# Kernel tuning notes

Hardware: AMD Instinct MI355X
Metric: run time of the kernel (lower is better)

The kernel has to match this reference:

```python
import jax, jax.numpy as jnp
import numpy as np

NUM_HEADS = 8
WINDOW = 64
ENCODERS = 6
EPS = 1e-5


def _positional_encoding(S, D, dtype=jnp.float32):
    pos = jnp.arange(S, dtype=jnp.float32)[:, None]
    div = jnp.exp(-jnp.log(10000.0) * jnp.arange(0, D, 2, dtype=jnp.float32) / D)
    ang = pos * div  # [S, D/2]
    pe = jnp.zeros((S, D), dtype=jnp.float32)
    pe = pe.at[:, 0::2].set(jnp.sin(ang)).at[:, 1::2].set(jnp.cos(ang))
    return pe.astype(dtype)


def _layernorm(x, g, b):
    mu = jnp.mean(x, axis=-1, keepdims=True)
    var = jnp.var(x, axis=-1, keepdims=True)
    return (x - mu) * jax.lax.rsqrt(var + EPS) * g + b


def _local_attention(x, wq, bq, wk, bk, wv, bv, window_mask):
    B, S, D = x.shape
    Dh = D // NUM_HEADS
    scale = Dh ** -0.5
    def split(t):  # [B,S,D] -> [B,H,S,Dh]
        return t.reshape(B, S, NUM_HEADS, Dh).transpose(0, 2, 1, 3)
    q = split(x @ wq.T + bq)
    k = split(x @ wk.T + bk)
    v = split(x @ wv.T + bv)
    scores = jnp.einsum('bhqd,bhkd->bhqk', q, k)
    # FAITHFUL: out-of-window entries are ZERO (not -inf); softmax over full S.
    scores = jnp.where(window_mask, scores, 0.0) * scale
    probs = jax.nn.softmax(scores, axis=-1)
    out = jnp.einsum('bhqk,bhkd->bhqd', probs, v)
    return out.transpose(0, 2, 1, 3).reshape(B, S, D)


def reference(inputs, emb, wq, bq, wk, bk, wv, bv, ln_g, ln_b,
              fc1_w, fc1_b, fc2_w, fc2_b, out_w, out_b):
    B, S = inputs.shape
    D = emb.shape[1]
    # window slice in torch source: [max(0, i-W), min(S, i+W))  (end exclusive)
    i = jnp.arange(S)[:, None]
    j = jnp.arange(S)[None, :]
    window_mask = (j >= i - WINDOW) & (j < i + WINDOW)  # [S, S]

    x = emb[inputs]  # [B, S, D]
    x = x + _positional_encoding(S, D, x.dtype)
    for _ in range(ENCODERS):  # shared weights across encoder iterations
        a = _local_attention(x, wq, bq, wk, bk, wv, bv, window_mask)
        x = _layernorm(a, ln_g, ln_b)
        h = jax.nn.relu(x @ fc1_w.T + fc1_b)
        x = (h @ fc2_w.T + fc2_b) + x
        x = _layernorm(x, ln_g, ln_b)
    x = x.reshape(B, S * D)
    return x @ out_w.T + out_b


def setup_inputs() -> dict:
    key = jax.random.key(0)
    ks = jax.random.split(key, 16)
    B, S, D, Hd, V, C = 8, 1024, 512, 2048, 32000, 6
    s = 0.02
    return {
        'inputs': jax.random.randint(ks[0], (B, S), 0, 31999),
        'emb': jax.random.normal(ks[1], (V, D), jnp.float32) * s,
        'wq': jax.random.normal(ks[2], (D, D), jnp.float32) * s,
        'bq': jnp.zeros((D,), jnp.float32),
        'wk': jax.random.normal(ks[3], (D, D), jnp.float32) * s,
        'bk': jnp.zeros((D,), jnp.float32),
        'wv': jax.random.normal(ks[4], (D, D), jnp.float32) * s,
        'bv': jnp.zeros((D,), jnp.float32),
        'ln_g': jnp.ones((D,), jnp.float32),
        'ln_b': jnp.zeros((D,), jnp.float32),
        'fc1_w': jax.random.normal(ks[5], (Hd, D), jnp.float32) * s,
        'fc1_b': jnp.zeros((Hd,), jnp.float32),
        'fc2_w': jax.random.normal(ks[6], (D, Hd), jnp.float32) * s,
        'fc2_b': jnp.zeros((D,), jnp.float32),
        'out_w': jax.random.normal(ks[7], (C, S * D), jnp.float32) * s,
        'out_b': jnp.zeros((C,), jnp.float32),
    }
```

## Files before the change

### kernel.cpp

```cpp
#include <hip/hip_runtime.h>

#define S_LEN 1024
#define DMODEL 512
#define NHEADS 8
#define DHEAD 64
#define HDIM 2048
#define WIN 64

typedef _Float16 f16x8 __attribute__((ext_vector_type(8)));
typedef _Float16 f16x2 __attribute__((ext_vector_type(2)));
typedef float f32x4 __attribute__((ext_vector_type(4)));
typedef float f32x16 __attribute__((ext_vector_type(16)));

__device__ __forceinline__ void stage16(const _Float16* g, _Float16* l) {
  __builtin_amdgcn_global_load_lds((const __attribute__((address_space(1))) unsigned int*)g,
                                   (__attribute__((address_space(3))) unsigned int*)l, 16, 0, 0);
}

__global__ void wprep_kernel(const float* __restrict__ wq, const float* __restrict__ wk,
                             const float* __restrict__ wv, const float* __restrict__ bq,
                             const float* __restrict__ bk, const float* __restrict__ bv,
                             const float* __restrict__ w1, const float* __restrict__ w2,
                             const float* __restrict__ wo,
                             _Float16* __restrict__ Wqkv, float* __restrict__ bqkv,
                             _Float16* __restrict__ W1h, _Float16* __restrict__ W2h,
                             _Float16* __restrict__ Woh) {
  int i = blockIdx.x * 256 + threadIdx.x;
  if (i < 262144) {
    Wqkv[i]          = (_Float16)wq[i];
    Wqkv[262144 + i] = (_Float16)wk[i];
    Wqkv[524288 + i] = (_Float16)wv[i];
  }
  if (i < 1048576) {
    W1h[i] = (_Float16)w1[i];
    W2h[i] = (_Float16)w2[i];
    Woh[i]           = (_Float16)wo[i];
    Woh[1048576 + i] = (_Float16)wo[1048576 + i];
    Woh[2097152 + i] = (_Float16)wo[2097152 + i];
  }
  if (i < 512) { bqkv[i] = bq[i]; bqkv[512 + i] = bk[i]; bqkv[1024 + i] = bv[i]; }
}

__global__ void embed_pe_kernel(const int* __restrict__ inputs, const float* __restrict__ emb,
                                _Float16* __restrict__ Xb) {
  int row = blockIdx.x;
  int s = row & (S_LEN - 1);
  int t = threadIdx.x;
  int tok = inputs[row];
  float dv = __expf(-logf(10000.0f) * (2.0f * (float)t) / (float)DMODEL);
  float ang = (float)s * dv;
  float sv = sinf(ang);
  float cv = cosf(ang);
  size_t base = (size_t)row * DMODEL + 2 * t;
  float x0 = emb[(size_t)tok * DMODEL + 2 * t] + sv;
  float x1 = emb[(size_t)tok * DMODEL + 2 * t + 1] + cv;
  f16x2 h; h[0] = (_Float16)x0; h[1] = (_Float16)x1;
  *(f16x2*)(Xb + base) = h;
}

#define EPI_RELU16 1
#define EPI_QKV 3
#define EPI_PART 4

template <int EPI>
__launch_bounds__(256)
__global__ void mfma_gemm(const _Float16* __restrict__ A, const _Float16* __restrict__ W,
                          const float* __restrict__ bias,
                          float* __restrict__ Cf0, float* __restrict__ Cf1,
                          _Float16* __restrict__ Ch, float* __restrict__ VS,
                          int M, int N, int Kstride, int Kslice) {
  __shared__ _Float16 As[2][128 * 32];
  __shared__ _Float16 Bs[2][128 * 32];
  const int bm = blockIdx.x * 128;
  const int bn = blockIdx.y * 128;
  const int z = blockIdx.z;
  const int t = threadIdx.x;
  const int lane = t & 63;
  const int w = t >> 6;
  const int wr = w >> 1, wc = w & 1;
  const int l15 = lane & 15, l4 = lane >> 4;

  const int idx0 = t, idx1 = t + 256;
  const int r0 = idx0 >> 2, kg0 = (idx0 & 3) << 3;
  const int r1 = idx1 >> 2, kg1 = (idx1 & 3) << 3;
  const _Float16* Ag0 = A + (size_t)(bm + r0) * Kstride + kg0;
  const _Float16* Ag1 = A + (size_t)(bm + r1) * Kstride + kg1;
  const _Float16* Wg0 = W + (size_t)(bn + r0) * Kstride + kg0;
  const _Float16* Wg1 = W + (size_t)(bn + r1) * Kstride + kg1;

  const int kbeg = z * Kslice;
  const int nsteps = Kslice >> 5;

  stage16(Ag0 + kbeg, As[0] + idx0 * 8);
  stage16(Ag1 + kbeg, As[0] + idx1 * 8);
  stage16(Wg0 + kbeg, Bs[0] + idx0 * 8);
  stage16(Wg1 + kbeg, Bs[0] + idx1 * 8);
  __syncthreads();

  f32x4 acc[4][4] = {};
  int cur = 0;
  for (int s = 0; s < nsteps; ++s) {
    if (s + 1 < nsteps) {
      int kn = kbeg + (s + 1) * 32;
      stage16(Ag0 + kn, As[cur ^ 1] + idx0 * 8);
      stage16(Ag1 + kn, As[cur ^ 1] + idx1 * 8);
      stage16(Wg0 + kn, Bs[cur ^ 1] + idx0 * 8);
      stage16(Wg1 + kn, Bs[cur ^ 1] + idx1 * 8);
    }
    f16x8 af[4], bf[4];
#pragma unroll
    for (int m = 0; m < 4; ++m)
      af[m] = *(const f16x8*)&As[cur][(wr * 64 + m * 16 + l15) * 32 + l4 * 8];
#pragma unroll
    for (int n = 0; n < 4; ++n)
      bf[n] = *(const f16x8*)&Bs[cur][(wc * 64 + n * 16 + l15) * 32 + l4 * 8];
#pragma unroll
    for (int m = 0; m < 4; ++m)
#pragma unroll
      for (int n = 0; n < 4; ++n)
        acc[m][n] = __builtin_amdgcn_mfma_f32_16x16x32_f16(af[m], bf[n], acc[m][n], 0, 0, 0);
    __syncthreads();
    cur ^= 1;
  }

  float* dst = (EPI == EPI_PART) ? (z ? Cf1 : Cf0) : Cf0;
  float cs[4] = {0.f, 0.f, 0.f, 0.f};
#pragma unroll
  for (int n = 0; n < 4; ++n) {
    int col = bn + wc * 64 + n * 16 + l15;
    float bb = (EPI == EPI_PART) ? 0.f : bias[col];
#pragma unroll
    for (int m = 0; m < 4; ++m) {
      int row = bm + wr * 64 + m * 16 + l4 * 4;
#pragma unroll
      for (int j = 0; j < 4; ++j) {
        float v = acc[m][n][j] + bb;
        if (EPI == EPI_RELU16) {
          v = fmaxf(v, 0.0f);
          Ch[(size_t)(row + j) * N + col] = (_Float16)v;
        } else if (EPI == EPI_QKV) {
          Ch[(size_t)(row + j) * N + col] = (_Float16)v;
          cs[n] += v;
        } else {
          dst[(size_t)(row + j) * N + col] = v;
        }
      }
    }
  }
  if (EPI == EPI_QKV && bn >= 1024) {
    const int batch = bm >> 10;
#pragma unroll
    for (int n = 0; n < 4; ++n) {
      float s = cs[n];
      s += __shfl_xor(s, 16);
      s += __shfl_xor(s, 32);
      if (l4 == 0) {
        int col = bn + wc * 64 + n * 16 + l15;
        atomicAdd(&VS[batch * 512 + (col - 1024)], s);
      }
    }
  }
}

__global__ void vs_zero_kernel(float* __restrict__ VS) {
  VS[blockIdx.x * 256 + threadIdx.x] = 0.0f;
}

#define KTMAX 256
#define VTS 264

__launch_bounds__(256)
__global__ void attn_kernel(const _Float16* __restrict__ QKVh, const float* __restrict__ VSg,
                            float* __restrict__ O) {
  __shared__ _Float16 Ks[KTMAX * 64];
  __shared__ _Float16 Vt[64 * VTS];
  __shared__ float VsC[8][64];

  const int qb0 = blockIdx.x * 128, h = blockIdx.y, b = blockIdx.z;
  const int jlo = max(0, qb0 - WIN);
  const int jhi = min(S_LEN, qb0 + 128 + WIN);
  const int KT = jhi - jlo;
  const int t = threadIdx.x;
  const int lane = t & 63, w = t >> 6;
  const int hi = lane >> 5, l31 = lane & 31;

  const _Float16* Kg = QKVh + ((size_t)(b * S_LEN + jlo)) * 1536 + 512 + h * 64;
#pragma unroll
  for (int p = 0; p < 8; ++p) {
    int u = t + p * 256;
    int row = u >> 3;
    int cb = (u & 7) * 16;
    int rowc = min(row, KT - 1);
    int scb = cb ^ ((row & 7) << 4);
    stage16(Kg + (size_t)rowc * 1536 + (scb >> 1), Ks + u * 8);
  }
  const _Float16* Vg = QKVh + ((size_t)(b * S_LEN + jlo)) * 1536 + 1024 + h * 64;
#pragma unroll
  for (int p = 0; p < 8; ++p) {
    int u = t + p * 256;
    int row = u >> 3;
    int d0 = (u & 7) * 8;
    f16x8 v = {0, 0, 0, 0, 0, 0, 0, 0};
    if (row < KT) v = *(const f16x8*)(Vg + (size_t)row * 1536 + d0);
#pragma unroll
    for (int e = 0; e < 8; ++e) Vt[(d0 + e) * VTS + row] = v[e];
  }
  __syncthreads();
  for (int slot = t; slot < 512; slot += 256) {
    int c = slot >> 6, d = slot & 63;
    const f16x8* col = (const f16x8*)(Vt + d * VTS + c * 32);
    float s = 0.f;
#pragma unroll
    for (int g = 0; g < 4; ++g) {
      f16x8 v = col[g];
#pragma unroll
      for (int e = 0; e < 8; ++e) s += (float)v[e];
    }
    VsC[c][d] = s;
  }
  const int qw = qb0 + w * 32;
  const _Float16* Qg = QKVh + ((size_t)(b * S_LEN + qw + l31)) * 1536 + h * 64;
  f16x8 qf[4];
#pragma unroll
  for (int ds = 0; ds < 4; ++ds) qf[ds] = *(const f16x8*)(Qg + ds * 16 + hi * 8);
  __syncthreads();

  const int c0 = max(0, qw - WIN - jlo) >> 5;
  const int c1 = min(KT, qw + 96 - jlo) >> 5;
  const int nproc = (c1 - c0) * 32;
  const int i = qw + l31;
  const int wlo = i - WIN, whi = i + WIN;

  float m = 0.f, l = 0.f;
  f32x16 accA = {}, accB = {};

  union PK { f16x2 h; unsigned u; };
  union A8 { unsigned u[4]; f16x8 h; };

  for (int c = c0; c < c1; ++c) {
    const int kb = c * 32;
    f32x16 sf = {};
#pragma unroll
    for (int ds = 0; ds < 4; ++ds) {
      int row = kb + l31;
      int cbyte = ((ds * 16 + hi * 8) * 2) ^ ((row & 7) << 4);
      f16x8 kf = *(const f16x8*)((const char*)Ks + row * 128 + cbyte);
      sf = __builtin_amdgcn_mfma_f32_32x32x16_f16(kf, qf[ds], sf, 0, 0, 0);
    }
    float s[16]; float pm = -1e30f;
#pragma unroll
    for (int r = 0; r < 16; ++r) {
      int gk = jlo + kb + (r & 3) + 8 * (r >> 2) + 4 * hi;
      float v = (gk >= wlo && gk < whi) ? sf[r] * 0.125f : 0.f;
      s[r] = v;
      pm = fmaxf(pm, v);
    }
    pm = fmaxf(pm, __shfl_xor(pm, 32));
    if (!__all(pm <= m + 8.f)) {
      float mn = fmaxf(m, pm);
      float f = __expf(m - mn);
      l *= f;
#pragma unroll
      for (int r = 0; r < 16; ++r) {
        int q = (r & 3) + 8 * (r >> 2) + 4 * hi;
        float fr = __shfl(f, q);
        accA[r] *= fr; accB[r] *= fr;
      }
      m = mn;
    }
    float p[16]; float ls = 0.f;
#pragma unroll
    for (int r = 0; r < 16; ++r) { p[r] = __expf(s[r] - m); ls += p[r]; }
    l += ls;
    unsigned u[8], x[8];
#pragma unroll
    for (int kk = 0; kk < 8; ++kk) {
      PK cv; cv.h[0] = (_Float16)p[2 * kk]; cv.h[1] = (_Float16)p[2 * kk + 1];
      u[kk] = cv.u;
    }
#pragma unroll
    for (int kk = 0; kk < 8; ++kk) x[kk] = (unsigned)__shfl_xor((int)u[kk], 32);
    A8 a0, a1;
    a0.u[0] = hi ? x[2] : u[0]; a0.u[1] = hi ? x[3] : u[1];
    a0.u[2] = hi ? u[2] : x[0]; a0.u[3] = hi ? u[3] : x[1];
    a1.u[0] = hi ? x[6] : u[4]; a1.u[1] = hi ? x[7] : u[5];
    a1.u[2] = hi ? u[6] : x[4]; a1.u[3] = hi ? u[7] : x[5];
#pragma unroll
    for (int ks = 0; ks < 2; ++ks) {
      f16x8 pa = ks ? a1.h : a0.h;
      f16x8 v0 = *(const f16x8*)(Vt + (size_t)(l31) * VTS + kb + ks * 16 + hi * 8);
      f16x8 v1 = *(const f16x8*)(Vt + (size_t)(32 + l31) * VTS + kb + ks * 16 + hi * 8);
      accA = __builtin_amdgcn_mfma_f32_32x32x16_f16(pa, v0, accA, 0, 0, 0);
      accB = __builtin_amdgcn_mfma_f32_32x32x16_f16(pa, v1, accB, 0, 0, 0);
    }
  }

  l = l + __shfl_xor(l, 32);
  const int dA = l31, dB = 32 + l31;
  float vsA = 0.f, vsB = 0.f;
  for (int c = c0; c < c1; ++c) { vsA += VsC[c][dA]; vsB += VsC[c][dB]; }
  const float vtA = VSg[b * 512 + h * 64 + dA];
  const float vtB = VSg[b * 512 + h * 64 + dB];
  const float zcount = (float)(S_LEN - nproc);
#pragma unroll
  for (int r = 0; r < 16; ++r) {
    int q = (r & 3) + 8 * (r >> 2) + 4 * hi;
    float mq = __shfl(m, q);
    float lq = __shfl(l, q);
    float em = __expf(-mq);
    float denom = lq + zcount * em;
    float inv = 1.0f / denom;
    size_t rowbase = ((size_t)(b * S_LEN + qw + q)) * DMODEL + h * 64;
    O[rowbase + dA] = (accA[r] + em * (vtA - vsA)) * inv;
    O[rowbase + dB] = (accB[r] + em * (vtB - vsB)) * inv;
  }
}

__global__ void ln_kernel(const float* __restrict__ X, const float* __restrict__ g,
                          const float* __restrict__ be, float* __restrict__ Y,
                          _Float16* __restrict__ Yh) {
  int row = blockIdx.x;
  int t = threadIdx.x;
  const float* x = X + (size_t)row * DMODEL;
  float2 v = *(const float2*)(x + 2 * t);
  float s = v.x + v.y;
  float sq = v.x * v.x + v.y * v.y;
#pragma unroll
  for (int off = 32; off; off >>= 1) {
    s += __shfl_xor(s, off);
    sq += __shfl_xor(sq, off);
  }
  __shared__ float ss[4], sqq[4];
  int w = t >> 6, lane = t & 63;
  if (lane == 0) { ss[w] = s; sqq[w] = sq; }
  __syncthreads();
  s = ss[0] + ss[1] + ss[2] + ss[3];
  sq = sqq[0] + sqq[1] + sqq[2] + sqq[3];
  float mu = s * (1.0f / DMODEL);
  float var = sq * (1.0f / DMODEL) - mu * mu;
  float rstd = rsqrtf(var + 1e-5f);
  float g0 = g[2 * t], g1 = g[2 * t + 1];
  float b0 = be[2 * t], b1 = be[2 * t + 1];
  float2 o;
  o.x = (v.x - mu) * rstd * g0 + b0;
  o.y = (v.y - mu) * rstd * g1 + b1;
  *(float2*)(Y + (size_t)row * DMODEL + 2 * t) = o;
  f16x2 hh; hh[0] = (_Float16)o.x; hh[1] = (_Float16)o.y;
  *(f16x2*)(Yh + (size_t)row * DMODEL + 2 * t) = hh;
}

__global__ void ln2_fused_kernel(const float* __restrict__ P0, const float* __restrict__ P1,
                                 const float* __restrict__ XB, const float* __restrict__ fb,
                                 const float* __restrict__ g, const float* __restrict__ be,
                                 _Float16* __restrict__ Yh) {
  int row = blockIdx.x;
  int t = threadIdx.x;
  size_t off = (size_t)row * DMODEL + 2 * t;
  float2 p0 = *(const float2*)(P0 + off);
  float2 p1 = *(const float2*)(P1 + off);
  float2 xb = *(const float2*)(XB + off);
  float2 v;
  v.x = p0.x + p1.x + fb[2 * t]     + xb.x;
  v.y = p0.y + p1.y + fb[2 * t + 1] + xb.y;
  float s = v.x + v.y;
  float sq = v.x * v.x + v.y * v.y;
#pragma unroll
  for (int off2 = 32; off2; off2 >>= 1) {
    s += __shfl_xor(s, off2);
    sq += __shfl_xor(sq, off2);
  }
  __shared__ float ss[4], sqq[4];
  int w = t >> 6, lane = t & 63;
  if (lane == 0) { ss[w] = s; sqq[w] = sq; }
  __syncthreads();
  s = ss[0] + ss[1] + ss[2] + ss[3];
  sq = sqq[0] + sqq[1] + sqq[2] + sqq[3];
  float mu = s * (1.0f / DMODEL);
  float var = sq * (1.0f / DMODEL) - mu * mu;
  float rstd = rsqrtf(var + 1e-5f);
  float g0 = g[2 * t], g1 = g[2 * t + 1];
  float b0 = be[2 * t], b1 = be[2 * t + 1];
  f16x2 hh;
  hh[0] = (_Float16)((v.x - mu) * rstd * g0 + b0);
  hh[1] = (_Float16)((v.y - mu) * rstd * g1 + b1);
  *(f16x2*)(Yh + off) = hh;
}

__global__ void outproj_partial_kernel(const _Float16* __restrict__ Xb,
                                       const _Float16* __restrict__ Woh,
                                       float* __restrict__ part) {
  const int KTOT = S_LEN * DMODEL;
  const int CH = KTOT / 32;
  int chunk = blockIdx.x, c = blockIdx.y, b = blockIdx.z;
  const int t = threadIdx.x;
  const _Float16* x = Xb + (size_t)b * KTOT + (size_t)chunk * CH;
  const _Float16* wv = Woh + (size_t)c * KTOT + (size_t)chunk * CH;
  float acc = 0.f;
#pragma unroll
  for (int p = 0; p < 8; ++p) {
    f16x8 a = *(const f16x8*)(x + (p * 256 + t) * 8);
    f16x8 w8 = *(const f16x8*)(wv + (p * 256 + t) * 8);
#pragma unroll
    for (int e = 0; e < 8; ++e) acc += (float)a[e] * (float)w8[e];
  }
#pragma unroll
  for (int off = 32; off; off >>= 1) acc += __shfl_xor(acc, off);
  __shared__ float red[4];
  int w = t >> 6, lane = t & 63;
  if (lane == 0) red[w] = acc;
  __syncthreads();
  if (t == 0)
    part[(b * 6 + c) * 32 + chunk] = red[0] + red[1] + red[2] + red[3];
}

__global__ void outproj_final_kernel(const float* __restrict__ part, const float* __restrict__ ob,
                                     float* __restrict__ out) {
  int idx = threadIdx.x;
  if (idx < 48) {
    float s = 0.f;
#pragma unroll
    for (int k = 0; k < 32; ++k) s += part[idx * 32 + k];
    out[idx] = s + ob[idx % 6];
  }
}

extern "C" void kernel_launch(void* const* d_in, const int* in_sizes, int n_in,
                              void* d_out, int out_size, void* d_ws, size_t ws_size,
                              hipStream_t stream) {
  (void)in_sizes; (void)n_in; (void)out_size; (void)ws_size;
  const int*   inputs = (const int*)  d_in[0];
  const float* emb    = (const float*)d_in[1];
  const float* wq     = (const float*)d_in[2];
  const float* bq     = (const float*)d_in[3];
  const float* wk     = (const float*)d_in[4];
  const float* bk     = (const float*)d_in[5];
  const float* wv     = (const float*)d_in[6];
  const float* bv     = (const float*)d_in[7];
  const float* ln_g   = (const float*)d_in[8];
  const float* ln_b   = (const float*)d_in[9];
  const float* fc1_w  = (const float*)d_in[10];
  const float* fc1_b  = (const float*)d_in[11];
  const float* fc2_w  = (const float*)d_in[12];
  const float* fc2_b  = (const float*)d_in[13];
  const float* out_w  = (const float*)d_in[14];
  const float* out_b  = (const float*)d_in[15];
  float* out = (float*)d_out;

  const int M = 8192;
  char* p = (char*)d_ws;
  float*    P0   = (float*)p;      p += (size_t)M * 512 * 4;
  _Float16* Xb   = (_Float16*)p;   p += (size_t)M * 512 * 2;
  _Float16* QKVh = (_Float16*)p;   p += (size_t)M * 1536 * 2;
  float*    XB   = (float*)p;      p += (size_t)M * 512 * 4;
  _Float16* XBb  = (_Float16*)p;   p += (size_t)M * 512 * 2;
  _Float16* H    = (_Float16*)p;   p += (size_t)M * 2048 * 2;
  float*    Ab   = (float*)H;
  _Float16* Wqkv = (_Float16*)p;   p += (size_t)1536 * 512 * 2;
  _Float16* W1h  = (_Float16*)p;   p += (size_t)2048 * 512 * 2;
  _Float16* W2h  = (_Float16*)p;   p += (size_t)512 * 2048 * 2;
  _Float16* Woh  = (_Float16*)p;   p += (size_t)6 * 524288 * 2;
  float*    bqkv = (float*)p;      p += 1536 * 4;
  float*    VS   = (float*)p;      p += 4096 * 4;
  float*    part = (float*)p;      p += 1536 * 4;
  float*    P1   = (float*)QKVh;

  wprep_kernel<<<4096, 256, 0, stream>>>(wq, wk, wv, bq, bk, bv, fc1_w, fc2_w, out_w,
                                         Wqkv, bqkv, W1h, W2h, Woh);
  embed_pe_kernel<<<8192, 256, 0, stream>>>(inputs, emb, Xb);
  for (int it = 0; it < 6; ++it) {
    vs_zero_kernel<<<16, 256, 0, stream>>>(VS);
    mfma_gemm<EPI_QKV><<<dim3(64, 12), 256, 0, stream>>>(Xb, Wqkv, bqkv, nullptr, nullptr,
                                                         QKVh, VS, M, 1536, 512, 512);
    attn_kernel<<<dim3(8, 8, 8), 256, 0, stream>>>(QKVh, VS, Ab);
    ln_kernel<<<8192, 256, 0, stream>>>(Ab, ln_g, ln_b, XB, XBb);
    mfma_gemm<EPI_RELU16><<<dim3(64, 16), 256, 0, stream>>>(XBb, W1h, fc1_b, nullptr, nullptr,
                                                            H, nullptr, M, 2048, 512, 512);
    mfma_gemm<EPI_PART><<<dim3(64, 4, 2), 256, 0, stream>>>(H, W2h, nullptr, P0, P1,
                                                            nullptr, nullptr, M, 512, 2048, 1024);
    ln2_fused_kernel<<<8192, 256, 0, stream>>>(P0, P1, XB, fc2_b, ln_g, ln_b, Xb);
  }
  outproj_partial_kernel<<<dim3(32, 6, 8), 256, 0, stream>>>(Xb, Woh, part);
  outproj_final_kernel<<<1, 64, 0, stream>>>(part, out_b, out);
}
```

Baseline: 782.9 us.

## Replace 128x128 GEMM with 256x256 swizzled-LDS 8-wave GEMM and fold VS zeroing

Replaces the 128x128 tile, K=32, 4-wave MFMA GEMM with a 256x256 tile, K=64, 8-wave kernel. It uses XOR-swizzled LDS layout and staged loads interleaved across four compute phases with explicit waitcnt/barrier and setprio. FC2 now uses a 4-way split-K, with two partials written in fp16 into reused buffers and summed in ln2. The separate VS zeroing kernel is folded into the embed and ln2 kernels. This aims for more data reuse per tile and fewer launches, at the cost of fewer blocks, fp16 rounding of some partial sums, and fragile manual synchronisation.

Result: slower. 936.8 us (+19.7%).

```diff
diff --git a/kernel.cpp b/kernel.cpp
--- a/kernel.cpp
+++ b/kernel.cpp
@@ -42,10 +42,11 @@
 }
 
 __global__ void embed_pe_kernel(const int* __restrict__ inputs, const float* __restrict__ emb,
-                                _Float16* __restrict__ Xb) {
+                                _Float16* __restrict__ Xb, float* __restrict__ VS) {
   int row = blockIdx.x;
   int s = row & (S_LEN - 1);
   int t = threadIdx.x;
+  if (row < 16) VS[row * 256 + t] = 0.0f;
   int tok = inputs[row];
   float dv = __expf(-logf(10000.0f) * (2.0f * (float)t) / (float)DMODEL);
   float ang = (float)s * dv;
@@ -63,86 +64,111 @@
 #define EPI_PART 4
 
 template <int EPI>
-__launch_bounds__(256)
-__global__ void mfma_gemm(const _Float16* __restrict__ A, const _Float16* __restrict__ W,
-                          const float* __restrict__ bias,
-                          float* __restrict__ Cf0, float* __restrict__ Cf1,
-                          _Float16* __restrict__ Ch, float* __restrict__ VS,
-                          int M, int N, int Kstride, int Kslice) {
-  __shared__ _Float16 As[2][128 * 32];
-  __shared__ _Float16 Bs[2][128 * 32];
-  const int bm = blockIdx.x * 128;
-  const int bn = blockIdx.y * 128;
+__launch_bounds__(512, 2)
+__global__ void gemm256(const _Float16* __restrict__ A, const _Float16* __restrict__ W,
+                        const float* __restrict__ bias,
+                        float* __restrict__ Pf0, float* __restrict__ Pf1,
+                        _Float16* __restrict__ Ph2, _Float16* __restrict__ Ph3,
+                        _Float16* __restrict__ Ch, float* __restrict__ VS,
+                        int N, int Kstride, int Kslice) {
+  __shared__ _Float16 As[2][16384];
+  __shared__ _Float16 Bs[2][16384];
+  const int bm = blockIdx.x * 256;
+  const int bn = blockIdx.y * 256;
   const int z = blockIdx.z;
   const int t = threadIdx.x;
   const int lane = t & 63;
   const int w = t >> 6;
-  const int wr = w >> 1, wc = w & 1;
+  const int wm = w >> 2, wn = w & 3;
   const int l15 = lane & 15, l4 = lane >> 4;
-
-  const int idx0 = t, idx1 = t + 256;
-  const int r0 = idx0 >> 2, kg0 = (idx0 & 3) << 3;
-  const int r1 = idx1 >> 2, kg1 = (idx1 & 3) << 3;
-  const _Float16* Ag0 = A + (size_t)(bm + r0) * Kstride + kg0;
-  const _Float16* Ag1 = A + (size_t)(bm + r1) * Kstride + kg1;
-  const _Float16* Wg0 = W + (size_t)(bn + r0) * Kstride + kg0;
-  const _Float16* Wg1 = W + (size_t)(bn + r1) * Kstride + kg1;
-
   const int kbeg = z * Kslice;
-  const int nsteps = Kslice >> 5;
-
-  stage16(Ag0 + kbeg, As[0] + idx0 * 8);
-  stage16(Ag1 + kbeg, As[0] + idx1 * 8);
-  stage16(Wg0 + kbeg, Bs[0] + idx0 * 8);
-  stage16(Wg1 + kbeg, Bs[0] + idx1 * 8);
-  __syncthreads();
-
-  f32x4 acc[4][4] = {};
-  int cur = 0;
-  for (int s = 0; s < nsteps; ++s) {
-    if (s + 1 < nsteps) {
-      int kn = kbeg + (s + 1) * 32;
-      stage16(Ag0 + kn, As[cur ^ 1] + idx0 * 8);
-      stage16(Ag1 + kn, As[cur ^ 1] + idx1 * 8);
-      stage16(Wg0 + kn, Bs[cur ^ 1] + idx0 * 8);
-      stage16(Wg1 + kn, Bs[cur ^ 1] + idx1 * 8);
-    }
-    f16x8 af[4], bf[4];
-#pragma unroll
-    for (int m = 0; m < 4; ++m)
-      af[m] = *(const f16x8*)&As[cur][(wr * 64 + m * 16 + l15) * 32 + l4 * 8];
-#pragma unroll
-    for (int n = 0; n < 4; ++n)
-      bf[n] = *(const f16x8*)&Bs[cur][(wc * 64 + n * 16 + l15) * 32 + l4 * 8];
-#pragma unroll
-    for (int m = 0; m < 4; ++m)
-#pragma unroll
-      for (int n = 0; n < 4; ++n)
-        acc[m][n] = __builtin_amdgcn_mfma_f32_16x16x32_f16(af[m], bf[n], acc[m][n], 0, 0, 0);
-    __syncthreads();
-    cur ^= 1;
-  }
-
-  float* dst = (EPI == EPI_PART) ? (z ? Cf1 : Cf0) : Cf0;
+  const int NT = Kslice >> 6;
+
+  auto stA = [&](int h, int i, int s2, int kof) {
+    int hr = i * 64 + (t >> 3);
+    int row = h * 64 + ((hr < 64) ? hr : hr + 64);
+    int c = t & 7, gc = c ^ (row & 7);
+    stage16(A + (size_t)(bm + row) * Kstride + kof + gc * 8, &As[s2][row * 64 + c * 8]);
+  };
+  auto stB = [&](int h, int i, int s2, int kof) {
+    int hr = i * 64 + (t >> 3);
+    int row = ((hr >> 5) << 6) + h * 32 + (hr & 31);
+    int c = t & 7, gc = c ^ (row & 7);
+    stage16(W + (size_t)(bn + row) * Kstride + kof + gc * 8, &Bs[s2][row * 64 + c * 8]);
+  };
+
+  stA(0, 0, 0, kbeg); stA(0, 1, 0, kbeg);
+  stB(0, 0, 0, kbeg); stB(0, 1, 0, kbeg);
+  stB(1, 0, 0, kbeg); stB(1, 1, 0, kbeg);
+  stA(1, 0, 0, kbeg); stA(1, 1, 0, kbeg);
+
+  f32x4 acc[8][4] = {};
+  for (int tt = 0; tt < NT; ++tt) {
+    const int s = tt & 1, s2 = s ^ 1;
+    const int tn = (tt + 1 < NT) ? tt + 1 : NT - 1;
+    const int kofn = kbeg + tn * 64;
+#pragma unroll
+    for (int p = 0; p < 4; ++p) {
+      if (p < 3) asm volatile("s_waitcnt vmcnt(4)" ::: "memory");
+      asm volatile("s_barrier" ::: "memory");
+      if (p == 0)      { stA(0, 0, s2, kofn); stA(0, 1, s2, kofn); }
+      else if (p == 1) { stB(0, 0, s2, kofn); stB(0, 1, s2, kofn); }
+      else if (p == 2) { stB(1, 0, s2, kofn); stB(1, 1, s2, kofn); }
+      else             { stA(1, 0, s2, kofn); stA(1, 1, s2, kofn); }
+      const int qa = p >> 1, qb = p & 1;
+      f16x8 af[4][2], bf[2][2];
+#pragma unroll
+      for (int mf = 0; mf < 4; ++mf) {
+        int row = wm * 128 + qa * 64 + mf * 16 + l15;
+        int rx = row & 7;
+#pragma unroll
+        for (int ks = 0; ks < 2; ++ks)
+          af[mf][ks] = *(const f16x8*)&As[s][row * 64 + ((ks * 4 + l4) ^ rx) * 8];
+      }
+#pragma unroll
+      for (int nf = 0; nf < 2; ++nf) {
+        int row = wn * 64 + qb * 32 + nf * 16 + l15;
+        int rx = row & 7;
+#pragma unroll
+        for (int ks = 0; ks < 2; ++ks)
+          bf[nf][ks] = *(const f16x8*)&Bs[s][row * 64 + ((ks * 4 + l4) ^ rx) * 8];
+      }
+      __builtin_amdgcn_s_setprio(1);
+#pragma unroll
+      for (int mf = 0; mf < 4; ++mf)
+#pragma unroll
+        for (int nf = 0; nf < 2; ++nf) {
+          acc[qa * 4 + mf][qb * 2 + nf] = __builtin_amdgcn_mfma_f32_16x16x32_f16(
+              af[mf][0], bf[nf][0], acc[qa * 4 + mf][qb * 2 + nf], 0, 0, 0);
+          acc[qa * 4 + mf][qb * 2 + nf] = __builtin_amdgcn_mfma_f32_16x16x32_f16(
+              af[mf][1], bf[nf][1], acc[qa * 4 + mf][qb * 2 + nf], 0, 0, 0);
+        }
+      __builtin_amdgcn_s_setprio(0);
+    }
+  }
+
   float cs[4] = {0.f, 0.f, 0.f, 0.f};
 #pragma unroll
   for (int n = 0; n < 4; ++n) {
-    int col = bn + wc * 64 + n * 16 + l15;
+    int col = bn + wn * 64 + n * 16 + l15;
     float bb = (EPI == EPI_PART) ? 0.f : bias[col];
 #pragma unroll
-    for (int m = 0; m < 4; ++m) {
-      int row = bm + wr * 64 + m * 16 + l4 * 4;
+    for (int m = 0; m < 8; ++m) {
+      int row0 = bm + wm * 128 + m * 16 + l4 * 4;
 #pragma unroll
       for (int j = 0; j < 4; ++j) {
         float v = acc[m][n][j] + bb;
+        size_t off = (size_t)(row0 + j) * N + col;
         if (EPI == EPI_RELU16) {
-          v = fmaxf(v, 0.0f);
-          Ch[(size_t)(row + j) * N + col] = (_Float16)v;
+          Ch[off] = (_Float16)fmaxf(v, 0.0f);
         } else if (EPI == EPI_QKV) {
-          Ch[(size_t)(row + j) * N + col] = (_Float16)v;
+          Ch[off] = (_Float16)v;
           cs[n] += v;
         } else {
-          dst[(size_t)(row + j) * N + col] = v;
+          if (z == 0) Pf0[off] = v;
+          else if (z == 1) Pf1[off] = v;
+          else if (z == 2) Ph2[off] = (_Float16)v;
+          else Ph3[off] = (_Float16)v;
         }
       }
     }
@@ -151,19 +177,15 @@
     const int batch = bm >> 10;
 #pragma unroll
     for (int n = 0; n < 4; ++n) {
-      float s = cs[n];
-      s += __shfl_xor(s, 16);
-      s += __shfl_xor(s, 32);
+      float sv = cs[n];
+      sv += __shfl_xor(sv, 16);
+      sv += __shfl_xor(sv, 32);
       if (l4 == 0) {
-        int col = bn + wc * 64 + n * 16 + l15;
-        atomicAdd(&VS[batch * 512 + (col - 1024)], s);
+        int col = bn + wn * 64 + n * 16 + l15;
+        atomicAdd(&VS[batch * 512 + (col - 1024)], sv);
       }
     }
   }
-}
-
-__global__ void vs_zero_kernel(float* __restrict__ VS) {
-  VS[blockIdx.x * 256 + threadIdx.x] = 0.0f;
 }
 
 #define KTMAX 256
@@ -350,18 +372,22 @@
 }
 
 __global__ void ln2_fused_kernel(const float* __restrict__ P0, const float* __restrict__ P1,
+                                 const _Float16* __restrict__ P2h, const _Float16* __restrict__ P3h,
                                  const float* __restrict__ XB, const float* __restrict__ fb,
                                  const float* __restrict__ g, const float* __restrict__ be,
-                                 _Float16* __restrict__ Yh) {
+                                 _Float16* __restrict__ Yh, float* __restrict__ VS) {
   int row = blockIdx.x;
   int t = threadIdx.x;
+  if (row < 16) VS[row * 256 + t] = 0.0f;
   size_t off = (size_t)row * DMODEL + 2 * t;
   float2 p0 = *(const float2*)(P0 + off);
   float2 p1 = *(const float2*)(P1 + off);
+  f16x2 p2 = *(const f16x2*)(P2h + off);
+  f16x2 p3 = *(const f16x2*)(P3h + off);
   float2 xb = *(const float2*)(XB + off);
   float2 v;
-  v.x = p0.x + p1.x + fb[2 * t]     + xb.x;
-  v.y = p0.y + p1.y + fb[2 * t + 1] + xb.y;
+  v.x = p0.x + p1.x + (float)p2[0] + (float)p3[0] + fb[2 * t]     + xb.x;
+  v.y = p0.y + p1.y + (float)p2[1] + (float)p3[1] + fb[2 * t + 1] + xb.y;
   float s = v.x + v.y;
   float sq = v.x * v.x + v.y * v.y;
 #pragma unroll
@@ -446,14 +472,14 @@
   const float* out_b  = (const float*)d_in[15];
   float* out = (float*)d_out;
 
-  const int M = 8192;
+  const int M = 8192; (void)M;
   char* p = (char*)d_ws;
-  float*    P0   = (float*)p;      p += (size_t)M * 512 * 4;
-  _Float16* Xb   = (_Float16*)p;   p += (size_t)M * 512 * 2;
-  _Float16* QKVh = (_Float16*)p;   p += (size_t)M * 1536 * 2;
-  float*    XB   = (float*)p;      p += (size_t)M * 512 * 4;
-  _Float16* XBb  = (_Float16*)p;   p += (size_t)M * 512 * 2;
-  _Float16* H    = (_Float16*)p;   p += (size_t)M * 2048 * 2;
+  float*    P0   = (float*)p;      p += (size_t)8192 * 512 * 4;
+  _Float16* Xb   = (_Float16*)p;   p += (size_t)8192 * 512 * 2;
+  _Float16* QKVh = (_Float16*)p;   p += (size_t)8192 * 1536 * 2;
+  float*    XB   = (float*)p;      p += (size_t)8192 * 512 * 4;
+  _Float16* XBb  = (_Float16*)p;   p += (size_t)8192 * 512 * 2;
+  _Float16* H    = (_Float16*)p;   p += (size_t)8192 * 2048 * 2;
   float*    Ab   = (float*)H;
   _Float16* Wqkv = (_Float16*)p;   p += (size_t)1536 * 512 * 2;
   _Float16* W1h  = (_Float16*)p;   p += (size_t)2048 * 512 * 2;
@@ -463,21 +489,23 @@
   float*    VS   = (float*)p;      p += 4096 * 4;
   float*    part = (float*)p;      p += 1536 * 4;
   float*    P1   = (float*)QKVh;
+  _Float16* P2   = Xb;
+  _Float16* P3   = XBb;
 
   wprep_kernel<<<4096, 256, 0, stream>>>(wq, wk, wv, bq, bk, bv, fc1_w, fc2_w, out_w,
                                          Wqkv, bqkv, W1h, W2h, Woh);
-  embed_pe_kernel<<<8192, 256, 0, stream>>>(inputs, emb, Xb);
+  embed_pe_kernel<<<8192, 256, 0, stream>>>(inputs, emb, Xb, VS);
   for (int it = 0; it < 6; ++it) {
-    vs_zero_kernel<<<16, 256, 0, stream>>>(VS);
-    mfma_gemm<EPI_QKV><<<dim3(64, 12), 256, 0, stream>>>(Xb, Wqkv, bqkv, nullptr, nullptr,
-                                                         QKVh, VS, M, 1536, 512, 512);
+    gemm256<EPI_QKV><<<dim3(32, 6), 512, 0, stream>>>(Xb, Wqkv, bqkv,
+        nullptr, nullptr, nullptr, nullptr, QKVh, VS, 1536, 512, 512);
     attn_kernel<<<dim3(8, 8, 8), 256, 0, stream>>>(QKVh, VS, Ab);
     ln_kernel<<<8192, 256, 0, stream>>>(Ab, ln_g, ln_b, XB, XBb);
-    mfma_gemm<EPI_RELU16><<<dim3(64, 16), 256, 0, stream>>>(XBb, W1h, fc1_b, nullptr, nullptr,
-                                                            H, nullptr, M, 2048, 512, 512);
-    mfma_gemm<EPI_PART><<<dim3(64, 4, 2), 256, 0, stream>>>(H, W2h, nullptr, P0, P1,
-                                                            nullptr, nullptr, M, 512, 2048, 1024);
-    ln2_fused_kernel<<<8192, 256, 0, stream>>>(P0, P1, XB, fc2_b, ln_g, ln_b, Xb);
+    gemm256<EPI_RELU16><<<dim3(32, 8), 512, 0, stream>>>(XBb, W1h, fc1_b,
+        nullptr, nullptr, nullptr, nullptr, H, nullptr, 2048, 512, 512);
+    gemm256<EPI_PART><<<dim3(32, 2, 4), 512, 0, stream>>>(H, W2h, nullptr,
+        P0, P1, P2, P3, nullptr, nullptr, 512, 2048, 512);
+    ln2_fused_kernel<<<8192, 256, 0, stream>>>(P0, P1, P2, P3, XB, fc2_b,
+                                               ln_g, ln_b, Xb, VS);
   }
   outproj_partial_kernel<<<dim3(32, 6, 8), 256, 0, stream>>>(Xb, Woh, part);
   outproj_final_kernel<<<1, 64, 0, stream>>>(part, out_b, out);
```
